# Optimization experiments

Measured on AMD Instinct MI355X. Metric: run time of the kernel, lower is better.

Reference implementation:

```python
import jax, jax.numpy as jnp
import numpy as np

B, N, L, D = 4, 16, 2048, 512


def setup_inputs() -> dict:
    key = jax.random.key(0)
    k1, k2, k3, k4 = jax.random.split(key, 4)
    scale = 1.0 / np.sqrt(D)
    return {
        "x": jax.random.normal(k1, (B, N, L, D), dtype=jnp.float32),
        "highway": jax.random.normal(k2, (B, L, D), dtype=jnp.float32),
        "Wq": jax.random.normal(k3, (D, D), dtype=jnp.float32) * scale,
        "bq": jnp.zeros((D,), dtype=jnp.float32),
        "Wk": jax.random.normal(k4, (D, D), dtype=jnp.float32) * scale,
        "bk": jnp.zeros((D,), dtype=jnp.float32),
    }


def reference(x, highway, Wq, bq, Wk, bk):
    # x: (B,N,L,D), highway: (B,L,D)
    d = x.shape[-1]
    q = highway @ Wq.T + bq                       # (B,L,D)
    k = x @ Wk.T + bk                             # (B,N,L,D)
    scores = jnp.einsum('bld,bnld->bln', q, k) / jnp.sqrt(jnp.float32(d))
    weights = jax.nn.softmax(scores, axis=-1)     # softmax over neurons N
    x_pooled = jnp.einsum('bln,bnld->bld', weights, x)
    return x_pooled
```

## Files before the change

kernel.cpp:

```cpp
#include <hip/hip_runtime.h>
#include <hip/hip_bf16.h>

#define Bb 4
#define Nn 16
#define Ll 2048
#define Dd 512

template <bool BT, bool BIAS>
__global__ __launch_bounds__(256) void gemm_f32(const float* __restrict__ A,
                                                const float* __restrict__ Bm,
                                                const float* __restrict__ bias,
                                                float* __restrict__ C) {
    const int K = 512;
    __shared__ float As[16][128];
    __shared__ float Bs[16][128];
    const int m0 = blockIdx.x * 128;
    const int n0 = blockIdx.y * 128;
    const int tid = threadIdx.x;
    const int tr = tid >> 4;
    const int tc = tid & 15;

    float acc[8][8];
#pragma unroll
    for (int i = 0; i < 8; i++)
#pragma unroll
        for (int j = 0; j < 8; j++) acc[i][j] = 0.f;

    for (int k0 = 0; k0 < K; k0 += 16) {
#pragma unroll
        for (int i = 0; i < 2; i++) {
            int f = tid + i * 256;
            int row = f >> 2;
            int c4 = (f & 3) * 4;
            float4 v = *(const float4*)&A[(size_t)(m0 + row) * K + k0 + c4];
            As[c4 + 0][row] = v.x;
            As[c4 + 1][row] = v.y;
            As[c4 + 2][row] = v.z;
            As[c4 + 3][row] = v.w;
        }
        if (!BT) {
#pragma unroll
            for (int i = 0; i < 2; i++) {
                int f = tid + i * 256;
                int row = f >> 5;
                int c4 = (f & 31) * 4;
                float4 v = *(const float4*)&Bm[(size_t)(k0 + row) * 512 + n0 + c4];
                *(float4*)&Bs[row][c4] = v;
            }
        } else {
#pragma unroll
            for (int i = 0; i < 2; i++) {
                int f = tid + i * 256;
                int row = f >> 2;
                int c4 = (f & 3) * 4;
                float4 v = *(const float4*)&Bm[(size_t)(n0 + row) * 512 + k0 + c4];
                Bs[c4 + 0][row] = v.x;
                Bs[c4 + 1][row] = v.y;
                Bs[c4 + 2][row] = v.z;
                Bs[c4 + 3][row] = v.w;
            }
        }
        __syncthreads();
#pragma unroll
        for (int k = 0; k < 16; k++) {
            float a[8], bb[8];
            *(float4*)&a[0] = *(const float4*)&As[k][tr * 8];
            *(float4*)&a[4] = *(const float4*)&As[k][tr * 8 + 4];
            *(float4*)&bb[0] = *(const float4*)&Bs[k][tc * 8];
            *(float4*)&bb[4] = *(const float4*)&Bs[k][tc * 8 + 4];
#pragma unroll
            for (int i = 0; i < 8; i++)
#pragma unroll
                for (int j = 0; j < 8; j++) acc[i][j] += a[i] * bb[j];
        }
        __syncthreads();
    }

#pragma unroll
    for (int i = 0; i < 8; i++) {
        int row = m0 + tr * 8 + i;
#pragma unroll
        for (int j = 0; j < 8; j += 4) {
            int col = n0 + tc * 8 + j;
            float4 v = {acc[i][j], acc[i][j + 1], acc[i][j + 2], acc[i][j + 3]};
            if (BIAS) {
                v.x += bias[col + 0];
                v.y += bias[col + 1];
                v.z += bias[col + 2];
                v.w += bias[col + 3];
            }
            *(float4*)&C[(size_t)row * 512 + col] = v;
        }
    }
}

__global__ __launch_bounds__(256) void pool_kernel(const float* __restrict__ x,
                                                   const float* __restrict__ r,
                                                   float* __restrict__ out) {
    __shared__ float xs[Nn][Dd];
    __shared__ float s_s[Nn];
    const int row = blockIdx.x;
    const int b = row >> 11;
    const int l = row & (Ll - 1);
    const int tid = threadIdx.x;
    const int wv = tid >> 6;
    const int lane = tid & 63;

    const float4* rp = (const float4*)(r + (size_t)row * Dd);
    float4 rA = rp[lane];
    float4 rB = rp[lane + 64];

#pragma unroll
    for (int i = 0; i < 4; i++) {
        int n = wv * 4 + i;
        const float4* xp = (const float4*)(x + (((size_t)(b * Nn + n) * Ll) + l) * Dd);
        float4 v0 = xp[lane];
        float4 v1 = xp[lane + 64];
        *(float4*)&xs[n][lane * 4] = v0;
        *(float4*)&xs[n][256 + lane * 4] = v1;
        float acc = v0.x * rA.x + v0.y * rA.y + v0.z * rA.z + v0.w * rA.w +
                    v1.x * rB.x + v1.y * rB.y + v1.z * rB.z + v1.w * rB.w;
#pragma unroll
        for (int off = 32; off >= 1; off >>= 1) acc += __shfl_xor(acc, off);
        if (lane == 0) s_s[n] = acc * 0.04419417382415922f;
    }
    __syncthreads();

    float w[Nn];
    float m = s_s[0];
#pragma unroll
    for (int n = 1; n < Nn; n++) m = fmaxf(m, s_s[n]);
    float sum = 0.f;
#pragma unroll
    for (int n = 0; n < Nn; n++) {
        w[n] = __expf(s_s[n] - m);
        sum += w[n];
    }
    const float inv = 1.0f / sum;

    float acc0 = 0.f, acc1 = 0.f;
#pragma unroll
    for (int n = 0; n < Nn; n++) {
        float wn = w[n] * inv;
        acc0 += wn * xs[n][tid];
        acc1 += wn * xs[n][tid + 256];
    }
    out[(size_t)row * Dd + tid] = acc0;
    out[(size_t)row * Dd + tid + 256] = acc1;
}

extern "C" void kernel_launch(void* const* d_in, const int* in_sizes, int n_in,
                              void* d_out, int out_size, void* d_ws, size_t ws_size,
                              hipStream_t stream) {
    const float* x = (const float*)d_in[0];
    const float* highway = (const float*)d_in[1];
    const float* Wq = (const float*)d_in[2];
    const float* bq = (const float*)d_in[3];
    const float* Wk = (const float*)d_in[4];

    float* out = (float*)d_out;
    float* q = out;
    float* rbuf = (float*)d_ws;

    const int M = Bb * Ll;
    dim3 g1(M / 128, 512 / 128);

    gemm_f32<true, true><<<g1, 256, 0, stream>>>(highway, Wq, bq, q);
    gemm_f32<false, false><<<g1, 256, 0, stream>>>(q, Wk, nullptr, rbuf);
    pool_kernel<<<Bb * Ll, 256, 0, stream>>>(x, rbuf, out);
}
```

Measured before the change: 521.8 us.

## Precombine Wq^T·Wk into one weight and keep pooled x in registers

Instead of computing q = highway·Wq^T + bq and then r = q·Wk, the code precomputes Wc = Wq^T·Wk (512x512) and bc = bq·Wk. A single 8192x512x512 GEMM then yields r, replacing the second large GEMM with a small weight-only GEMM. The GEMM tile shrinks to 64x64 with K-step 32. The pool kernel now keeps its x rows in registers and reduces per-wave partial sums through a small shared buffer, rather than staging all 16 rows in 32KB of shared memory, which should raise occupancy. Precombining the weights changes floating-point rounding order slightly.

New measurement: 489.3 us. 1.07x faster.

```diff
diff --git a/kernel.cpp b/kernel.cpp
--- a/kernel.cpp
+++ b/kernel.cpp
@@ -6,98 +6,99 @@
 #define Ll 2048
 #define Dd 512
 
-template <bool BT, bool BIAS>
-__global__ __launch_bounds__(256) void gemm_f32(const float* __restrict__ A,
-                                                const float* __restrict__ Bm,
-                                                const float* __restrict__ bias,
-                                                float* __restrict__ C) {
-    const int K = 512;
-    __shared__ float As[16][128];
-    __shared__ float Bs[16][128];
-    const int m0 = blockIdx.x * 128;
-    const int n0 = blockIdx.y * 128;
+template <int TRANS_A, bool BIAS>
+__global__ __launch_bounds__(256) void gemm64(const float* __restrict__ A,
+                                              const float* __restrict__ Bm,
+                                              const float* __restrict__ bias,
+                                              float* __restrict__ C) {
+    __shared__ __align__(16) float As[32][68];
+    __shared__ __align__(16) float Bs[32][68];
+    const int m0 = blockIdx.x * 64;
+    const int n0 = blockIdx.y * 64;
     const int tid = threadIdx.x;
     const int tr = tid >> 4;
     const int tc = tid & 15;
 
-    float acc[8][8];
+    float acc[4][4];
 #pragma unroll
-    for (int i = 0; i < 8; i++)
+    for (int i = 0; i < 4; i++)
 #pragma unroll
-        for (int j = 0; j < 8; j++) acc[i][j] = 0.f;
+        for (int j = 0; j < 4; j++) acc[i][j] = 0.f;
 
-    for (int k0 = 0; k0 < K; k0 += 16) {
+    for (int k0 = 0; k0 < 512; k0 += 32) {
+        if (TRANS_A) {
 #pragma unroll
-        for (int i = 0; i < 2; i++) {
-            int f = tid + i * 256;
-            int row = f >> 2;
-            int c4 = (f & 3) * 4;
-            float4 v = *(const float4*)&A[(size_t)(m0 + row) * K + k0 + c4];
-            As[c4 + 0][row] = v.x;
-            As[c4 + 1][row] = v.y;
-            As[c4 + 2][row] = v.z;
-            As[c4 + 3][row] = v.w;
-        }
-        if (!BT) {
-#pragma unroll
-            for (int i = 0; i < 2; i++) {
-                int f = tid + i * 256;
-                int row = f >> 5;
-                int c4 = (f & 31) * 4;
-                float4 v = *(const float4*)&Bm[(size_t)(k0 + row) * 512 + n0 + c4];
-                *(float4*)&Bs[row][c4] = v;
+            for (int it = 0; it < 2; it++) {
+                int f = tid + it * 256;
+                int kk = f >> 4;
+                int c4 = (f & 15) * 4;
+                float4 v = *(const float4*)&A[(size_t)(k0 + kk) * 512 + m0 + c4];
+                *(float4*)&As[kk][c4] = v;
             }
         } else {
 #pragma unroll
-            for (int i = 0; i < 2; i++) {
-                int f = tid + i * 256;
-                int row = f >> 2;
-                int c4 = (f & 3) * 4;
-                float4 v = *(const float4*)&Bm[(size_t)(n0 + row) * 512 + k0 + c4];
-                Bs[c4 + 0][row] = v.x;
-                Bs[c4 + 1][row] = v.y;
-                Bs[c4 + 2][row] = v.z;
-                Bs[c4 + 3][row] = v.w;
+            for (int it = 0; it < 2; it++) {
+                int f = tid + it * 256;
+                int row = f >> 3;
+                int c4 = (f & 7) * 4;
+                float4 v = *(const float4*)&A[(size_t)(m0 + row) * 512 + k0 + c4];
+                As[c4 + 0][row] = v.x;
+                As[c4 + 1][row] = v.y;
+                As[c4 + 2][row] = v.z;
+                As[c4 + 3][row] = v.w;
             }
+        }
+#pragma unroll
+        for (int it = 0; it < 2; it++) {
+            int f = tid + it * 256;
+            int kk = f >> 4;
+            int c4 = (f & 15) * 4;
+            float4 v = *(const float4*)&Bm[(size_t)(k0 + kk) * 512 + n0 + c4];
+            *(float4*)&Bs[kk][c4] = v;
         }
         __syncthreads();
 #pragma unroll
-        for (int k = 0; k < 16; k++) {
-            float a[8], bb[8];
-            *(float4*)&a[0] = *(const float4*)&As[k][tr * 8];
-            *(float4*)&a[4] = *(const float4*)&As[k][tr * 8 + 4];
-            *(float4*)&bb[0] = *(const float4*)&Bs[k][tc * 8];
-            *(float4*)&bb[4] = *(const float4*)&Bs[k][tc * 8 + 4];
+        for (int k = 0; k < 32; k++) {
+            float a[4], b[4];
+            *(float4*)&a[0] = *(const float4*)&As[k][tr * 4];
+            *(float4*)&b[0] = *(const float4*)&Bs[k][tc * 4];
 #pragma unroll
-            for (int i = 0; i < 8; i++)
+            for (int i = 0; i < 4; i++)
 #pragma unroll
-                for (int j = 0; j < 8; j++) acc[i][j] += a[i] * bb[j];
+                for (int j = 0; j < 4; j++) acc[i][j] += a[i] * b[j];
         }
         __syncthreads();
     }
 
 #pragma unroll
-    for (int i = 0; i < 8; i++) {
-        int row = m0 + tr * 8 + i;
-#pragma unroll
-        for (int j = 0; j < 8; j += 4) {
-            int col = n0 + tc * 8 + j;
-            float4 v = {acc[i][j], acc[i][j + 1], acc[i][j + 2], acc[i][j + 3]};
-            if (BIAS) {
-                v.x += bias[col + 0];
-                v.y += bias[col + 1];
-                v.z += bias[col + 2];
-                v.w += bias[col + 3];
-            }
-            *(float4*)&C[(size_t)row * 512 + col] = v;
+    for (int i = 0; i < 4; i++) {
+        int row = m0 + tr * 4 + i;
+        int col = n0 + tc * 4;
+        float4 v = {acc[i][0], acc[i][1], acc[i][2], acc[i][3]};
+        if (BIAS) {
+            v.x += bias[col + 0];
+            v.y += bias[col + 1];
+            v.z += bias[col + 2];
+            v.w += bias[col + 3];
         }
+        *(float4*)&C[(size_t)row * 512 + col] = v;
     }
+}
+
+__global__ __launch_bounds__(256) void bc_kernel(const float* __restrict__ bq,
+                                                 const float* __restrict__ Wk,
+                                                 float* __restrict__ bc) {
+    int j = blockIdx.x * 256 + threadIdx.x;
+    float acc = 0.f;
+#pragma unroll 4
+    for (int k = 0; k < 512; k++) acc += bq[k] * Wk[(size_t)k * 512 + j];
+    bc[j] = acc;
 }
 
 __global__ __launch_bounds__(256) void pool_kernel(const float* __restrict__ x,
                                                    const float* __restrict__ r,
                                                    float* __restrict__ out) {
-    __shared__ float xs[Nn][Dd];
+    __shared__ __align__(16) float part[4][Dd];
     __shared__ float s_s[Nn];
     const int row = blockIdx.x;
     const int b = row >> 11;
@@ -110,43 +111,57 @@
     float4 rA = rp[lane];
     float4 rB = rp[lane + 64];
 
-#pragma unroll
-    for (int i = 0; i < 4; i++) {
-        int n = wv * 4 + i;
-        const float4* xp = (const float4*)(x + (((size_t)(b * Nn + n) * Ll) + l) * Dd);
-        float4 v0 = xp[lane];
-        float4 v1 = xp[lane + 64];
-        *(float4*)&xs[n][lane * 4] = v0;
-        *(float4*)&xs[n][256 + lane * 4] = v1;
-        float acc = v0.x * rA.x + v0.y * rA.y + v0.z * rA.z + v0.w * rA.w +
-                    v1.x * rB.x + v1.y * rB.y + v1.z * rB.z + v1.w * rB.w;
-#pragma unroll
-        for (int off = 32; off >= 1; off >>= 1) acc += __shfl_xor(acc, off);
-        if (lane == 0) s_s[n] = acc * 0.04419417382415922f;
+    float4 xv0_0, xv0_1, xv1_0, xv1_1, xv2_0, xv2_1, xv3_0, xv3_1;
+#define LOADDOT(I, VA, VB)                                                         \
+    {                                                                              \
+        int n = wv * 4 + I;                                                        \
+        const float4* xp =                                                         \
+            (const float4*)(x + (((size_t)(b * Nn + n) * Ll) + l) * Dd);           \
+        VA = xp[lane];                                                             \
+        VB = xp[lane + 64];                                                        \
+        float acc = VA.x * rA.x + VA.y * rA.y + VA.z * rA.z + VA.w * rA.w +        \
+                    VB.x * rB.x + VB.y * rB.y + VB.z * rB.z + VB.w * rB.w;         \
+        _Pragma("unroll") for (int off = 32; off >= 1; off >>= 1) acc +=           \
+            __shfl_xor(acc, off);                                                  \
+        if (lane == 0) s_s[n] = acc * 0.04419417382415922f;       \
     }
+    LOADDOT(0, xv0_0, xv0_1)
+    LOADDOT(1, xv1_0, xv1_1)
+    LOADDOT(2, xv2_0, xv2_1)
+    LOADDOT(3, xv3_0, xv3_1)
+#undef LOADDOT
     __syncthreads();
 
-    float w[Nn];
     float m = s_s[0];
 #pragma unroll
     for (int n = 1; n < Nn; n++) m = fmaxf(m, s_s[n]);
     float sum = 0.f;
 #pragma unroll
-    for (int n = 0; n < Nn; n++) {
-        w[n] = __expf(s_s[n] - m);
-        sum += w[n];
-    }
+    for (int n = 0; n < Nn; n++) sum += __expf(s_s[n] - m);
     const float inv = 1.0f / sum;
 
-    float acc0 = 0.f, acc1 = 0.f;
-#pragma unroll
-    for (int n = 0; n < Nn; n++) {
-        float wn = w[n] * inv;
-        acc0 += wn * xs[n][tid];
-        acc1 += wn * xs[n][tid + 256];
+    float4 p0 = {0.f, 0.f, 0.f, 0.f}, p1 = {0.f, 0.f, 0.f, 0.f};
+#define ACCW(I, VA, VB)                                                            \
+    {                                                                              \
+        float wn = __expf(s_s[wv * 4 + I] - m) * inv;                              \
+        p0.x += wn * VA.x; p0.y += wn * VA.y; p0.z += wn * VA.z; p0.w += wn * VA.w;\
+        p1.x += wn * VB.x; p1.y += wn * VB.y; p1.z += wn * VB.z; p1.w += wn * VB.w;\
     }
-    out[(size_t)row * Dd + tid] = acc0;
-    out[(size_t)row * Dd + tid + 256] = acc1;
+    ACCW(0, xv0_0, xv0_1)
+    ACCW(1, xv1_0, xv1_1)
+    ACCW(2, xv2_0, xv2_1)
+    ACCW(3, xv3_0, xv3_1)
+#undef ACCW
+
+    *(float4*)&part[wv][lane * 4] = p0;
+    *(float4*)&part[wv][256 + lane * 4] = p1;
+    __syncthreads();
+
+    float2 o;
+    o.x = part[0][2 * tid] + part[1][2 * tid] + part[2][2 * tid] + part[3][2 * tid];
+    o.y = part[0][2 * tid + 1] + part[1][2 * tid + 1] + part[2][2 * tid + 1] +
+          part[3][2 * tid + 1];
+    *(float2*)&out[(size_t)row * Dd + 2 * tid] = o;
 }
 
 extern "C" void kernel_launch(void* const* d_in, const int* in_sizes, int n_in,
@@ -159,13 +174,14 @@
     const float* Wk = (const float*)d_in[4];
 
     float* out = (float*)d_out;
-    float* q = out;
-    float* rbuf = (float*)d_ws;
+    float* Wc = (float*)d_ws;
+    float* bc = Wc + 512 * 512;
+    float* rbuf = bc + 512;
 
-    const int M = Bb * Ll;
-    dim3 g1(M / 128, 512 / 128);
-
-    gemm_f32<true, true><<<g1, 256, 0, stream>>>(highway, Wq, bq, q);
-    gemm_f32<false, false><<<g1, 256, 0, stream>>>(q, Wk, nullptr, rbuf);
+    dim3 gw(8, 8);
+    gemm64<1, false><<<gw, 256, 0, stream>>>(Wq, Wk, nullptr, Wc);
+    bc_kernel<<<2, 256, 0, stream>>>(bq, Wk, bc);
+    dim3 gr((Bb * Ll) / 64, 8);
+    gemm64<0, true><<<gr, 256, 0, stream>>>(highway, Wc, bc, rbuf);
     pool_kernel<<<Bb * Ll, 256, 0, stream>>>(x, rbuf, out);
 }
```
